# Kernel tuning notes

Hardware: AMD Instinct MI355X
Metric: run time of the kernel (lower is better)

Reference implementation:

```python
import jax, jax.numpy as jnp
import numpy as np

N, E, F, H, G, C = 50000, 800000, 128, 64, 512, 10
RATIO = 0.5  # forward arg `ratio` baked as constant


def seg_mean(msgs, idx, n):
    s = jax.ops.segment_sum(msgs, idx, num_segments=n)
    cnt = jax.ops.segment_sum(jnp.ones(idx.shape[0], msgs.dtype), idx, num_segments=n)
    return s / jnp.maximum(cnt, 1.0)[:, None]


def sage(x, src, dst, Wl, bl, Wr, ew=None):
    # PyG SAGEConv: lin_l(mean_{j->i} msg_j) + lin_r(x_i); weighted variant scales messages
    m = x[src] if ew is None else x[src] * ew[:, None]
    agg = seg_mean(m, dst, x.shape[0])
    return agg @ Wl + bl + x @ Wr


def topk_mask(scores, seg, num_graphs, ratio):
    # per-graph (segment) top-k edge selection: keep ceil(ratio*edges_in_graph) highest scores
    e = scores.shape[0]
    counts = jax.ops.segment_sum(jnp.ones(e, jnp.float32), seg, num_segments=num_graphs)
    order = jnp.lexsort((-scores, seg))  # sort by segment, then score descending
    seg_sorted = seg[order]
    starts = jnp.concatenate([jnp.zeros(1, jnp.float32), jnp.cumsum(counts)[:-1]])
    rank = jnp.arange(e, dtype=jnp.float32) - starts[seg_sorted]
    k = jnp.ceil(ratio * counts)
    sel = (rank < k[seg_sorted]).astype(scores.dtype)
    return jnp.zeros(e, scores.dtype).at[order].set(sel)


def setup_inputs():
    key = jax.random.key(0)
    ks = jax.random.split(key, 16)
    w = lambda k, shape, fan: (jax.random.normal(k, shape, jnp.float32) / np.sqrt(fan))
    return {
        'x': jax.random.normal(ks[0], (N, F), jnp.float32),
        'edge_index': jax.random.randint(ks[1], (2, E), 0, N, jnp.int32),
        'batch': jnp.sort(jax.random.randint(ks[2], (N,), 0, G, jnp.int32)),
        'W1l': w(ks[3], (F, H), F), 'b1l': jnp.zeros(H, jnp.float32), 'W1r': w(ks[4], (F, H), F),
        'W2l': w(ks[5], (H, H), H), 'b2l': jnp.zeros(H, jnp.float32), 'W2r': w(ks[6], (H, H), H),
        'W3l': w(ks[7], (H, H), H), 'b3l': jnp.zeros(H, jnp.float32), 'W3r': w(ks[8], (H, H), H),
        'Wlin1': w(ks[9], (H, H), H), 'blin1': jnp.zeros(H, jnp.float32),
        'Wlin2': w(ks[10], (H, C), H), 'blin2': jnp.zeros(C, jnp.float32),
    }


def reference(x, edge_index, batch, W1l, b1l, W1r, W2l, b2l, W2r, W3l, b3l, W3r, Wlin1, blin1, Wlin2, blin2):
    src, dst = edge_index[0], edge_index[1]
    h = jax.nn.relu(sage(x, src, dst, W1l, b1l, W1r))
    edge_scores = jnp.sum(h[src] * h[dst], axis=-1)  # [E]
    seg = batch[src]  # graph id per edge (sections)
    sampled = topk_mask(edge_scores, seg, G, RATIO)
    ew = edge_scores * sampled
    h = jax.nn.relu(sage(h, src, dst, W2l, b2l, W2r, ew))
    h = jax.nn.relu(sage(h, src, dst, W3l, b3l, W3r, ew))
    pooled = seg_mean(h, batch, G)  # global_mean_pool
    z = jax.nn.relu(pooled @ Wlin1 + blin1)
    z = z @ Wlin2 + blin2  # dropout inactive in eval
    return jax.nn.log_softmax(z, axis=-1), sampled
```

## Files before the change

kernel.cpp:

```cpp
#include <hip/hip_runtime.h>
#include <hip/hip_bf16.h>
#include <math.h>

static constexpr int N = 50000;
static constexpr int E = 800000;
static constexpr int F = 128;
static constexpr int H = 64;
static constexpr int G = 512;
static constexpr int C = 10;
static constexpr int CAP = 256;
static constexpr int NWIN = 8;
static constexpr int FILL_CH = 1280;
static constexpr int FB = E / FILL_CH;
static constexpr int DEGB = 256;
static constexpr int GB2 = (N + 31) / 32;
static constexpr int SB = E / 256;

static inline int cdiv(long a, int b) { return (int)((a + b - 1) / b); }

__device__ __forceinline__ float uinv_score(unsigned u) {
  return (u & 0x80000000u) ? __uint_as_float(u & 0x7fffffffu) : __uint_as_float(~u);
}

__device__ __forceinline__ int2 pack_slot(int s, int d, int g, int e) {
  unsigned a = (unsigned)s | ((unsigned)(d & 0x7FFF) << 17);
  unsigned b = ((unsigned)d >> 15) | ((unsigned)g << 2) | ((unsigned)e << 11);
  return make_int2((int)a, (int)b);
}
__device__ __forceinline__ int slot_src(int2 p) { return p.x & 0x1FFFF; }
__device__ __forceinline__ int slot_dst(int2 p) {
  return (int)(((unsigned)p.x >> 17) | (((unsigned)p.y & 3u) << 15));
}
__device__ __forceinline__ int slot_g(int2 p) { return (int)(((unsigned)p.y >> 2) & 0x1FFu); }
__device__ __forceinline__ int slot_eid(int2 p) { return (int)((unsigned)p.y >> 11); }

__global__ void k_deg_gemm(const int* __restrict__ dst, const int* __restrict__ batch,
                           int* __restrict__ deg, int* __restrict__ goff,
                           const float* __restrict__ x, const float* __restrict__ Wl,
                           const float* __restrict__ Wr, const float* __restrict__ bl,
                           float* __restrict__ y, float* __restrict__ r) {
  __shared__ float sx[16][F];
  int lane = threadIdx.x, ty = threadIdx.y;
  int tid = ty * 64 + lane;
  if (blockIdx.x >= DEGB) {
    int row0 = (blockIdx.x - DEGB) * 16;
    const float4* gsrc = (const float4*)(x + (size_t)row0 * F);
    float4* sdst = (float4*)(&sx[0][0]);
#pragma unroll
    for (int i = tid; i < 16 * F / 4; i += 256) sdst[i] = gsrc[i];
    __syncthreads();
    float al[4], ar[4];
    float bias = bl[lane];
#pragma unroll
    for (int j = 0; j < 4; ++j) { al[j] = 0.f; ar[j] = bias; }
#pragma unroll 4
    for (int f = 0; f < F; ++f) {
      float wl = Wl[f * H + lane];
      float wr = Wr[f * H + lane];
#pragma unroll
      for (int j = 0; j < 4; ++j) {
        float xv = sx[ty * 4 + j][f];
        al[j] += xv * wl;
        ar[j] += xv * wr;
      }
    }
#pragma unroll
    for (int j = 0; j < 4; ++j) {
      int row = row0 + ty * 4 + j;
      y[(size_t)row * H + lane] = al[j];
      r[(size_t)row * H + lane] = ar[j];
    }
    return;
  }
  for (int i = blockIdx.x * 256 + tid; i < N; i += DEGB * 256) {
    int b = batch[i];
    if (i == 0) {
      for (int g = 0; g <= b; ++g) goff[g] = 0;
    } else {
      int p = batch[i - 1];
      for (int g = p + 1; g <= b; ++g) goff[g] = i;
    }
    if (i == N - 1) {
      for (int g = b + 1; g <= G; ++g) goff[g] = N;
    }
  }
  const int4* d4 = (const int4*)dst;
  for (int i = blockIdx.x * 256 + tid; i < E / 4; i += DEGB * 256) {
    int4 v = d4[i];
    atomicAdd(&deg[v.x], 1);
    atomicAdd(&deg[v.y], 1);
    atomicAdd(&deg[v.z], 1);
    atomicAdd(&deg[v.w], 1);
  }
}

__global__ void k_scan_a(const int* __restrict__ cnt, int* __restrict__ off,
                         int* __restrict__ bsum, int n) {
  __shared__ int wsum[16];
  int tid = threadIdx.x, lane = tid & 63, wv = tid >> 6;
  int idx = blockIdx.x * 4096 + tid * 4;
  int v0 = (idx + 0 < n) ? cnt[idx + 0] : 0;
  int v1 = (idx + 1 < n) ? cnt[idx + 1] : 0;
  int v2 = (idx + 2 < n) ? cnt[idx + 2] : 0;
  int v3 = (idx + 3 < n) ? cnt[idx + 3] : 0;
  int local = v0 + v1 + v2 + v3;
  int inc = local;
  for (int d = 1; d < 64; d <<= 1) {
    int t = __shfl_up(inc, d);
    if (lane >= d) inc += t;
  }
  if (lane == 63) wsum[wv] = inc;
  __syncthreads();
  if (tid < 16) {
    int t = wsum[tid];
    for (int d = 1; d < 16; d <<= 1) {
      int u = __shfl_up(t, d);
      if (tid >= d) t += u;
    }
    wsum[tid] = t;
  }
  __syncthreads();
  int woff = (wv > 0) ? wsum[wv - 1] : 0;
  int excl = woff + inc - local;
  if (idx + 0 < n) off[idx + 0] = excl;
  if (idx + 1 < n) off[idx + 1] = excl + v0;
  if (idx + 2 < n) off[idx + 2] = excl + v0 + v1;
  if (idx + 3 < n) off[idx + 3] = excl + v0 + v1 + v2;
  if (tid == 0) bsum[blockIdx.x] = wsum[15];
}

__global__ void k_scan_c(int* __restrict__ off, int* __restrict__ cursor,
                         const int* __restrict__ bsum, int n, int nb) {
  __shared__ int spre[34];
  int tid = threadIdx.x;
  if (tid < 32) {
    int v = (tid < nb) ? bsum[tid] : 0;
    int inc = v;
    for (int d = 1; d < 32; d <<= 1) {
      int t = __shfl_up(inc, d);
      if (tid >= d) inc += t;
    }
    spre[tid] = inc - v;
  }
  __syncthreads();
  int i = blockIdx.x * 256 + tid;
  if (i < n) {
    int v = off[i] + spre[i >> 12];
    off[i] = v;
    cursor[i] = v;
  } else if (i == n) {
    off[n] = spre[nb];
  }
}

__global__ void k_fill(const int* __restrict__ src, const int* __restrict__ dst,
                       const int* __restrict__ batch, int* __restrict__ cursor,
                       int2* __restrict__ csrp, int* __restrict__ einv) {
  int win = blockIdx.x & 7;
  int chunk = blockIdx.x >> 3;
  int lo = win * (N / NWIN), hi = lo + (N / NWIN);
  int base = chunk * FILL_CH + threadIdx.x;
  int dd[FILL_CH / 256];
#pragma unroll
  for (int it = 0; it < FILL_CH / 256; ++it) dd[it] = dst[base + it * 256];
#pragma unroll
  for (int it = 0; it < FILL_CH / 256; ++it) {
    int d = dd[it];
    if (d >= lo && d < hi) {
      int e = base + it * 256;
      int s = src[e];
      int g = batch[s];
      int slot = atomicAdd(&cursor[d], 1);
      csrp[slot] = pack_slot(s, d, g, e);
      einv[e] = slot;
    }
  }
}

template <int K>
__global__ void k_gemm2h(const float* __restrict__ in, const float* __restrict__ Wl,
                         const float* __restrict__ Wr, const float* __restrict__ b,
                         __hip_bfloat16* __restrict__ y, float* __restrict__ r) {
  __shared__ float sx[16][K];
  int lane = threadIdx.x, ty = threadIdx.y;
  int tid = ty * 64 + lane;
  int row0 = blockIdx.x * 16;
  const float4* gsrc = (const float4*)(in + (size_t)row0 * K);
  float4* sdst = (float4*)(&sx[0][0]);
#pragma unroll
  for (int i = tid; i < 16 * K / 4; i += 256) sdst[i] = gsrc[i];
  __syncthreads();
  float al[4], ar[4];
  float bias = b[lane];
#pragma unroll
  for (int j = 0; j < 4; ++j) { al[j] = 0.f; ar[j] = bias; }
#pragma unroll 4
  for (int f = 0; f < K; ++f) {
    float wl = Wl[f * H + lane];
    float wr = Wr[f * H + lane];
#pragma unroll
    for (int j = 0; j < 4; ++j) {
      float xv = sx[ty * 4 + j][f];
      al[j] += xv * wl;
      ar[j] += xv * wr;
    }
  }
#pragma unroll
  for (int j = 0; j < 4; ++j) {
    int row = row0 + ty * 4 + j;
    y[(size_t)row * H + lane] = __float2bfloat16(al[j]);
    r[(size_t)row * H + lane] = ar[j];
  }
}

__global__ void k_agg1(const float* __restrict__ y, const float* __restrict__ r,
                       const int2* __restrict__ csrp, const int* __restrict__ off,
                       float* __restrict__ out) {
  int node = blockIdx.x * 8 + threadIdx.y;
  int lane = threadIdx.x;
  int q = lane >> 3, c = lane & 7;
  int s0 = off[node], s1 = off[node + 1];
  float4 a0 = make_float4(0.f, 0.f, 0.f, 0.f);
  float4 a1 = make_float4(0.f, 0.f, 0.f, 0.f);
  int i = s0 + q;
  for (; i + 8 < s1; i += 16) {
    int se0 = slot_src(csrp[i]);
    int se1 = slot_src(csrp[i + 8]);
    const float4* p0 = (const float4*)(y + (size_t)se0 * H);
    const float4* p1 = (const float4*)(y + (size_t)se1 * H);
    float4 u0 = p0[c], v0 = p0[c + 8];
    float4 u1 = p1[c], v1 = p1[c + 8];
    a0.x += u0.x + u1.x; a0.y += u0.y + u1.y; a0.z += u0.z + u1.z; a0.w += u0.w + u1.w;
    a1.x += v0.x + v1.x; a1.y += v0.y + v1.y; a1.z += v0.z + v1.z; a1.w += v0.w + v1.w;
  }
  for (; i < s1; i += 8) {
    int se = slot_src(csrp[i]);
    const float4* p = (const float4*)(y + (size_t)se * H);
    float4 u = p[c], v = p[c + 8];
    a0.x += u.x; a0.y += u.y; a0.z += u.z; a0.w += u.w;
    a1.x += v.x; a1.y += v.y; a1.z += v.z; a1.w += v.w;
  }
#pragma unroll
  for (int d = 8; d < 64; d <<= 1) {
    a0.x += __shfl_xor(a0.x, d); a0.y += __shfl_xor(a0.y, d);
    a0.z += __shfl_xor(a0.z, d); a0.w += __shfl_xor(a0.w, d);
    a1.x += __shfl_xor(a1.x, d); a1.y += __shfl_xor(a1.y, d);
    a1.w += __shfl_xor(a1.w, d); a1.z += __shfl_xor(a1.z, d);
  }
  if (q == 0) {
    float inv = 1.f / fmaxf((float)(s1 - s0), 1.f);
    const float4* rp = (const float4*)(r + (size_t)node * H);
    float4 r0 = rp[c], r1 = rp[c + 8];
    float4 o0, o1;
    o0.x = fmaxf(a0.x * inv + r0.x, 0.f); o0.y = fmaxf(a0.y * inv + r0.y, 0.f);
    o0.z = fmaxf(a0.z * inv + r0.z, 0.f); o0.w = fmaxf(a0.w * inv + r0.w, 0.f);
    o1.x = fmaxf(a1.x * inv + r1.x, 0.f); o1.y = fmaxf(a1.y * inv + r1.y, 0.f);
    o1.z = fmaxf(a1.z * inv + r1.z, 0.f); o1.w = fmaxf(a1.w * inv + r1.w, 0.f);
    float4* op = (float4*)(out + (size_t)node * H);
    op[c] = o0; op[c + 8] = o1;
  }
}

__global__ void k_agg_w(const __hip_bfloat16* __restrict__ y, const float* __restrict__ r,
                        const int2* __restrict__ csr2, const int* __restrict__ cnt2,
                        const int* __restrict__ off, float* __restrict__ out) {
  int node = blockIdx.x * 8 + threadIdx.y;
  int lane = threadIdx.x;
  int q = lane >> 3, c = lane & 7;
  int b0 = off[node], cn = cnt2[node];
  float a[8] = {0.f, 0.f, 0.f, 0.f, 0.f, 0.f, 0.f, 0.f};
  for (int j = q; j < cn; j += 8) {
    int2 sw = csr2[b0 + j];
    float w = __int_as_float(sw.y);
    uint4 pk = ((const uint4*)((const unsigned short*)y + (size_t)sw.x * H))[c];
    a[0] += w * __uint_as_float(pk.x << 16); a[1] += w * __uint_as_float(pk.x & 0xffff0000u);
    a[2] += w * __uint_as_float(pk.y << 16); a[3] += w * __uint_as_float(pk.y & 0xffff0000u);
    a[4] += w * __uint_as_float(pk.z << 16); a[5] += w * __uint_as_float(pk.z & 0xffff0000u);
    a[6] += w * __uint_as_float(pk.w << 16); a[7] += w * __uint_as_float(pk.w & 0xffff0000u);
  }
#pragma unroll
  for (int d = 8; d < 64; d <<= 1) {
#pragma unroll
    for (int j = 0; j < 8; ++j) a[j] += __shfl_xor(a[j], d);
  }
  if (q == 0) {
    int degn = off[node + 1] - off[node];
    float inv = 1.f / fmaxf((float)degn, 1.f);
    const float4* rp = (const float4*)(r + (size_t)node * H);
    float4 r0 = rp[2 * c], r1 = rp[2 * c + 1];
    float4 o0, o1;
    o0.x = fmaxf(a[0] * inv + r0.x, 0.f); o0.y = fmaxf(a[1] * inv + r0.y, 0.f);
    o0.z = fmaxf(a[2] * inv + r0.z, 0.f); o0.w = fmaxf(a[3] * inv + r0.w, 0.f);
    o1.x = fmaxf(a[4] * inv + r1.x, 0.f); o1.y = fmaxf(a[5] * inv + r1.y, 0.f);
    o1.z = fmaxf(a[6] * inv + r1.z, 0.f); o1.w = fmaxf(a[7] * inv + r1.w, 0.f);
    float4* op = (float4*)(out + (size_t)node * H);
    op[2 * c] = o0; op[2 * c + 1] = o1;
  }
}

__global__ void k_score_g2h(const float* __restrict__ h1, const int2* __restrict__ csrp,
                            unsigned* __restrict__ scoreu_csr,
                            unsigned short* __restrict__ seg_csr, int* __restrict__ hist,
                            const float* __restrict__ Wl, const float* __restrict__ Wr,
                            const float* __restrict__ bl,
                            __hip_bfloat16* __restrict__ y, float* __restrict__ r) {
  __shared__ float sx[32][H];
  int lane = threadIdx.x, ty = threadIdx.y;
  int q3 = blockIdx.x / 3, r3 = blockIdx.x - q3 * 3;
  if (r3 == 0 && q3 < GB2) {
    int tid = ty * 64 + lane;
    int row0 = q3 * 32;
    {
      int row = row0 + (tid >> 4);
      if (row < N)
        ((float4*)(&sx[0][0]))[tid] = ((const float4*)h1)[(size_t)row * (H / 4) + (tid & 15)];
    }
    __syncthreads();
    float al[4], ar[4];
    float bias = bl[lane];
#pragma unroll
    for (int j = 0; j < 4; ++j) { al[j] = 0.f; ar[j] = bias; }
#pragma unroll 4
    for (int f = 0; f < H; ++f) {
      float wl = Wl[f * H + lane];
      float wr = Wr[f * H + lane];
#pragma unroll
      for (int j = 0; j < 4; ++j) {
        float xv = sx[ty * 4 + j][f];
        al[j] += xv * wl;
        ar[j] += xv * wr;
      }
    }
#pragma unroll
    for (int j = 0; j < 4; ++j) {
      int row = row0 + ty * 4 + j;
      if (row < N) {
        y[(size_t)row * H + lane] = __float2bfloat16(al[j]);
        r[(size_t)row * H + lane] = ar[j];
      }
    }
  } else {
    int sid = blockIdx.x - (q3 + (r3 > 0 ? 1 : 0));
    int q = lane >> 4, c = lane & 15;
    int s = (sid * 8 + ty) * 32 + q * 8;
    int2 se[8];
#pragma unroll
    for (int j = 0; j < 8; ++j) se[j] = csrp[s + j];
    float4 xr[8], yr[8];
#pragma unroll
    for (int j = 0; j < 8; ++j)
      xr[j] = ((const float4*)(h1 + (size_t)slot_src(se[j]) * H))[c];
#pragma unroll
    for (int j = 0; j < 8; ++j)
      yr[j] = ((const float4*)(h1 + (size_t)slot_dst(se[j]) * H))[c];
    float p[8];
#pragma unroll
    for (int j = 0; j < 8; ++j)
      p[j] = yr[j].x * xr[j].x + yr[j].y * xr[j].y + yr[j].z * xr[j].z + yr[j].w * xr[j].w;
#pragma unroll
    for (int d = 1; d < 16; d <<= 1) {
#pragma unroll
      for (int j = 0; j < 8; ++j) p[j] += __shfl_xor(p[j], d);
    }
    if (c == 0) {
#pragma unroll
      for (int j = 0; j < 8; ++j) {
        int g = slot_g(se[j]);
        unsigned u = __float_as_uint(p[j]);
        u = (u & 0x80000000u) ? ~u : (u | 0x80000000u);
        scoreu_csr[s + j] = u;
        seg_csr[s + j] = (unsigned short)g;
        atomicAdd(&hist[g * 256 + (int)(u >> 24)], 1);
      }
    }
  }
}

__global__ void k_hist(const unsigned* __restrict__ scoreu, const unsigned short* __restrict__ seg,
                       const unsigned* __restrict__ prefix, int* __restrict__ hist, int pass) {
  int e = (blockIdx.x * 256 + threadIdx.x) * 4;
  if (e >= E) return;
  uint4 u4 = *(const uint4*)(scoreu + e);
  ushort4 s4 = *(const ushort4*)(seg + e);
  unsigned uu[4] = {u4.x, u4.y, u4.z, u4.w};
  int gg[4] = {(int)s4.x, (int)s4.y, (int)s4.z, (int)s4.w};
  int predshift = 32 - 8 * pass;
  int bshift = 24 - 8 * pass;
#pragma unroll
  for (int j = 0; j < 4; ++j) {
    unsigned u = uu[j];
    int g = gg[j];
    if ((u >> predshift) == (prefix[g] >> predshift))
      atomicAdd(&hist[g * 256 + (int)((u >> bshift) & 0xFFu)], 1);
  }
}

__global__ void k_scan(int* __restrict__ hist, unsigned* __restrict__ prefix,
                       int* __restrict__ krem, int pass) {
  int g = blockIdx.x;
  int lane = threadIdx.x;
  int4* row = (int4*)(hist + (size_t)g * 256);
  int4 v = row[lane];
  int vj[4] = {v.x, v.y, v.z, v.w};
  int s = v.x + v.y + v.z + v.w;
  int inc = s;
  for (int d = 1; d < 64; d <<= 1) {
    int t = __shfl_up(inc, d);
    if (lane >= d) inc += t;
  }
  int T = __shfl(inc, 63);
  int k = (pass == 0) ? ((T + 1) >> 1) : krem[g];
  int excl = inc - s;
  int pre[4] = {excl, excl + vj[0], excl + vj[0] + vj[1], excl + vj[0] + vj[1] + vj[2]};
  int bsel_l = -1, newk_l = 0;
  if (k > 0) {
    for (int j = 3; j >= 0; --j) {
      int suf = T - pre[j];
      if (suf >= k) { bsel_l = 4 * lane + j; newk_l = k - (suf - vj[j]); break; }
    }
  }
  unsigned long long mask = __ballot(bsel_l >= 0);
  int bsel = 255, newk = 0;
  if (k > 0 && mask) {
    int hi = 63 - __builtin_clzll(mask);
    bsel = __shfl(bsel_l, hi);
    newk = __shfl(newk_l, hi);
  }
  if (lane == 0) {
    unsigned base = (pass == 0) ? 0u : prefix[g];
    prefix[g] = base | ((unsigned)bsel << (24 - 8 * pass));
    krem[g] = newk;
  }
  row[lane] = make_int4(0, 0, 0, 0);
}

__global__ void k_select(const unsigned* __restrict__ scoreu_csr,
                         const unsigned short* __restrict__ seg_csr,
                         const unsigned* __restrict__ thresh,
                         int* __restrict__ eqcnt, int* __restrict__ eqlist,
                         unsigned char* __restrict__ sel_csr, float* __restrict__ ew_csr) {
  int s = (blockIdx.x * 256 + threadIdx.x) * 4;
  if (s >= E) return;
  uint4 u4 = *(const uint4*)(scoreu_csr + s);
  ushort4 g4 = *(const ushort4*)(seg_csr + s);
  unsigned uu[4] = {u4.x, u4.y, u4.z, u4.w};
  int gg[4] = {(int)g4.x, (int)g4.y, (int)g4.z, (int)g4.w};
  float ew[4];
  unsigned char sl[4];
#pragma unroll
  for (int j = 0; j < 4; ++j) {
    unsigned u = uu[j];
    int g = gg[j];
    unsigned t = thresh[g];
    unsigned um = u & 0xffffff00u;
    float sel = 0.f;
    if (um > t) sel = 1.f;
    else if (um == t) {
      int slot = atomicAdd(&eqcnt[g], 1);
      if (slot < CAP) eqlist[g * CAP + slot] = s + j;
    }
    sl[j] = (unsigned char)sel;
    ew[j] = uinv_score(u) * sel;
  }
  *(uchar4*)(sel_csr + s) = make_uchar4(sl[0], sl[1], sl[2], sl[3]);
  *(float4*)(ew_csr + s) = make_float4(ew[0], ew[1], ew[2], ew[3]);
}

__global__ void k_resolve(const int* __restrict__ krem, const int* __restrict__ eqcnt,
                          const int* __restrict__ eqlist, const int2* __restrict__ csrp,
                          const unsigned* __restrict__ scoreu_csr,
                          unsigned char* __restrict__ sel_csr, float* __restrict__ ew_csr) {
  int g = blockIdx.x * 256 + threadIdx.x;
  if (g >= G) return;
  int c = eqcnt[g]; if (c > CAP) c = CAP;
  int r = krem[g];  if (r > c) r = c;
  const int* lst = eqlist + g * CAP;
  unsigned last_u = 0u; int last_e = -1; bool first = true;
  for (int i = 0; i < r; ++i) {
    unsigned bu = 0u; int be = -1, bs = -1;
    for (int j = 0; j < c; ++j) {
      int slot = lst[j];
      unsigned u = scoreu_csr[slot];
      int eid = slot_eid(csrp[slot]);
      bool after = first || (u < last_u) || (u == last_u && eid > last_e);
      if (after && (bs < 0 || u > bu || (u == bu && eid < be))) { bu = u; be = eid; bs = slot; }
    }
    if (bs < 0) break;
    sel_csr[bs] = 1;
    ew_csr[bs] = uinv_score(bu);
    last_u = bu; last_e = be; first = false;
  }
}

__global__ void k_samp_comp(const unsigned char* __restrict__ sel,
                            const int2* __restrict__ csrp, const float* __restrict__ ewc,
                            const int* __restrict__ off, int2* __restrict__ csr2,
                            int* __restrict__ cnt2,
                            const int* __restrict__ einv, float* __restrict__ sampled) {
  int lane = threadIdx.x, ty = threadIdx.y;
  if (blockIdx.x < N / 8) {
    int node = blockIdx.x * 8 + ty;
    int s0 = off[node], s1 = off[node + 1];
    unsigned long long lt = ((unsigned long long)1 << lane) - 1;
    int cum = 0;
    for (int i0 = s0; i0 < s1; i0 += 64) {
      int i = i0 + lane;
      bool f = (i < s1) && sel[i];
      unsigned long long m = __ballot(f);
      if (f) {
        int rank = __popcll(m & lt);
        csr2[s0 + cum + rank] = make_int2(slot_src(csrp[i]), __float_as_int(ewc[i]));
      }
      cum += __popcll(m);
    }
    if (lane == 0) cnt2[node] = cum;
  } else {
    int tid = ty * 64 + lane;
    int e = ((blockIdx.x - N / 8) * 512 + tid) * 4;
    if (e >= E) return;
    int4 iv = *(const int4*)(einv + e);
    float4 o;
    o.x = (float)sel[iv.x];
    o.y = (float)sel[iv.y];
    o.z = (float)sel[iv.z];
    o.w = (float)sel[iv.w];
    *(float4*)(sampled + e) = o;
  }
}

__global__ void k_poolhead(const float* __restrict__ h3, const int* __restrict__ goff,
                           const float* __restrict__ W1, const float* __restrict__ b1,
                           const float* __restrict__ W2, const float* __restrict__ b2,
                           float* __restrict__ outp) {
  int g = blockIdx.x;
  int tid = threadIdx.x;
  int h = tid & 63, j = tid >> 6;
  int s0 = goff[g], s1 = goff[g + 1];
  float a = 0.f;
  for (int n = s0 + j; n < s1; n += 8) a += h3[(size_t)n * H + h];
  __shared__ float sp[8][H];
  __shared__ float p[H], z1[H], z2[C];
  __shared__ float lse;
  sp[j][h] = a;
  __syncthreads();
  if (j == 0) {
    float s = sp[0][h] + sp[1][h] + sp[2][h] + sp[3][h]
            + sp[4][h] + sp[5][h] + sp[6][h] + sp[7][h];
    float inv = 1.f / fmaxf((float)(s1 - s0), 1.f);
    p[h] = s * inv;
  }
  __syncthreads();
  if (j == 0) {
    float acc = b1[h];
#pragma unroll 8
    for (int f = 0; f < H; ++f) acc += p[f] * W1[f * H + h];
    z1[h] = fmaxf(acc, 0.f);
  }
  __syncthreads();
  if (tid < C) {
    float a2 = b2[tid];
#pragma unroll 8
    for (int f = 0; f < H; ++f) a2 += z1[f] * W2[f * C + tid];
    z2[tid] = a2;
  }
  __syncthreads();
  if (tid == 0) {
    float m = z2[0];
    for (int c = 1; c < C; ++c) m = fmaxf(m, z2[c]);
    float s = 0.f;
    for (int c = 0; c < C; ++c) s += expf(z2[c] - m);
    lse = m + logf(s);
  }
  __syncthreads();
  if (tid < C) outp[(size_t)g * C + tid] = z2[tid] - lse;
}

extern "C" void kernel_launch(void* const* d_in, const int* in_sizes, int n_in,
                              void* d_out, int out_size, void* d_ws, size_t ws_size,
                              hipStream_t stream) {
  const float* x     = (const float*)d_in[0];
  const int*   ei    = (const int*)d_in[1];
  const int*   batch = (const int*)d_in[2];
  const float* W1l   = (const float*)d_in[3];
  const float* b1l   = (const float*)d_in[4];
  const float* W1r   = (const float*)d_in[5];
  const float* W2l   = (const float*)d_in[6];
  const float* b2l   = (const float*)d_in[7];
  const float* W2r   = (const float*)d_in[8];
  const float* W3l   = (const float*)d_in[9];
  const float* b3l   = (const float*)d_in[10];
  const float* W3r   = (const float*)d_in[11];
  const float* Wlin1 = (const float*)d_in[12];
  const float* blin1 = (const float*)d_in[13];
  const float* Wlin2 = (const float*)d_in[14];
  const float* blin2 = (const float*)d_in[15];

  const int* srcv = ei;
  const int* dstv = ei + E;

  float* out_ls   = (float*)d_out;
  float* out_samp = out_ls + G * C;

  char* w = (char*)d_ws;
  auto carve = [&](size_t bytes) { void* p = (void*)w; w += (bytes + 255) & ~(size_t)255; return p; };
  char* zbase   = w;
  int*      deg     = (int*)carve((size_t)N * 4);
  int*      eqcnt   = (int*)carve((size_t)G * 4);
  int*      hist    = (int*)carve((size_t)G * 256 * 4);
  size_t    zbytes  = (size_t)(w - zbase);
  float*    h1      = (float*)carve((size_t)N * H * 4);
  float*    h2      = (float*)carve((size_t)N * H * 4);
  float*    h3      = (float*)carve((size_t)N * H * 4);
  float*    yb      = (float*)carve((size_t)N * H * 4);
  float*    rb      = (float*)carve((size_t)N * H * 4);
  __hip_bfloat16* ybh = (__hip_bfloat16*)carve((size_t)N * H * 2);
  unsigned* scoreu_csr = (unsigned*)carve((size_t)E * 4);
  unsigned short* seg_csr = (unsigned short*)carve((size_t)E * 2);
  float*    ew_csr     = (float*)carve((size_t)E * 4);
  unsigned char* sel_csr = (unsigned char*)carve((size_t)E);
  int2*     csrp    = (int2*)carve((size_t)E * 8);
  int*      einv    = (int*)carve((size_t)E * 4);
  int*      off     = (int*)carve((size_t)(N + 1) * 4);
  int*      cursor  = (int*)carve((size_t)N * 4);
  int*      cnt2    = (int*)carve((size_t)N * 4);
  int*      goff    = (int*)carve((size_t)(G + 1) * 4);
  unsigned* prefix  = (unsigned*)carve((size_t)G * 4);
  int*      krem    = (int*)carve((size_t)G * 4);
  int*      eqlist  = (int*)carve((size_t)G * CAP * 4);
  int*      bsum    = (int*)carve((size_t)16 * 4);
  int2*     csr2    = (int2*)carve((size_t)E * 8);

  hipMemsetAsync(zbase, 0, zbytes, stream);

  k_deg_gemm<<<DEGB + N / 16, dim3(64, 4), 0, stream>>>(dstv, batch, deg, goff,
                                                        x, W1l, W1r, b1l, yb, rb);
  int nb = cdiv(N, 4096);
  k_scan_a<<<nb, 1024, 0, stream>>>(deg, off, bsum, N);
  k_scan_c<<<cdiv(N + 1, 256), 256, 0, stream>>>(off, cursor, bsum, N, nb);

  k_fill<<<8 * FB, 256, 0, stream>>>(srcv, dstv, batch, cursor, csrp, einv);

  k_agg1<<<N / 8, dim3(64, 8), 0, stream>>>(yb, rb, csrp, off, h1);

  k_score_g2h<<<SB + GB2, dim3(64, 8), 0, stream>>>(h1, csrp, scoreu_csr, seg_csr, hist,
                                                    W2l, W2r, b2l, ybh, rb);
  k_scan<<<G, 64, 0, stream>>>(hist, prefix, krem, 0);
  for (int p = 1; p <= 2; ++p) {
    k_hist<<<cdiv(E / 4, 256), 256, 0, stream>>>(scoreu_csr, seg_csr, prefix, hist, p);
    k_scan<<<G, 64, 0, stream>>>(hist, prefix, krem, p);
  }
  k_select<<<cdiv(E / 4, 256), 256, 0, stream>>>(scoreu_csr, seg_csr, prefix,
                                                 eqcnt, eqlist, sel_csr, ew_csr);
  k_resolve<<<cdiv(G, 256), 256, 0, stream>>>(krem, eqcnt, eqlist, csrp, scoreu_csr,
                                              sel_csr, ew_csr);

  k_samp_comp<<<N / 8 + cdiv(E / 4, 512), dim3(64, 8), 0, stream>>>(
      sel_csr, csrp, ew_csr, off, csr2, cnt2, einv, out_samp);

  k_agg_w<<<N / 8, dim3(64, 8), 0, stream>>>(ybh, rb, csr2, cnt2, off, h2);

  k_gemm2h<H><<<N / 16, dim3(64, 4), 0, stream>>>(h2, W3l, W3r, b3l, ybh, rb);
  k_agg_w<<<N / 8, dim3(64, 8), 0, stream>>>(ybh, rb, csr2, cnt2, off, h3);

  k_poolhead<<<G, 512, 0, stream>>>(h3, goff, Wlin1, blin1, Wlin2, blin2, out_ls);
}
```

Measured before the change: 436.9 us.

## Move layer-1 GEMM into fill kernel and window degree atomics by dst range

The layer-1 dense GEMM blocks move out of the degree-count kernel and into the CSR fill kernel, so the GEMM runs alongside the atomic-heavy fill instead of the degree pass. The degree kernel now uses 512 blocks split into 8 destination windows, each block atomically incrementing only degrees in its window. The aim is to improve atomic locality and let the memory-bound fill overlap with compute. In exchange, each window rereads the whole dst array, and the fill kernel grows in size and shared-memory use.

```diff
diff --git a/kernel.cpp b/kernel.cpp
--- a/kernel.cpp
+++ b/kernel.cpp
@@ -12,7 +12,7 @@
 static constexpr int NWIN = 8;
 static constexpr int FILL_CH = 1280;
 static constexpr int FB = E / FILL_CH;
-static constexpr int DEGB = 256;
+static constexpr int DEGB = 512;
 static constexpr int GB2 = (N + 31) / 32;
 static constexpr int SB = E / 256;
 
@@ -34,44 +34,9 @@
 __device__ __forceinline__ int slot_g(int2 p) { return (int)(((unsigned)p.y >> 2) & 0x1FFu); }
 __device__ __forceinline__ int slot_eid(int2 p) { return (int)((unsigned)p.y >> 11); }
 
-__global__ void k_deg_gemm(const int* __restrict__ dst, const int* __restrict__ batch,
-                           int* __restrict__ deg, int* __restrict__ goff,
-                           const float* __restrict__ x, const float* __restrict__ Wl,
-                           const float* __restrict__ Wr, const float* __restrict__ bl,
-                           float* __restrict__ y, float* __restrict__ r) {
-  __shared__ float sx[16][F];
-  int lane = threadIdx.x, ty = threadIdx.y;
-  int tid = ty * 64 + lane;
-  if (blockIdx.x >= DEGB) {
-    int row0 = (blockIdx.x - DEGB) * 16;
-    const float4* gsrc = (const float4*)(x + (size_t)row0 * F);
-    float4* sdst = (float4*)(&sx[0][0]);
-#pragma unroll
-    for (int i = tid; i < 16 * F / 4; i += 256) sdst[i] = gsrc[i];
-    __syncthreads();
-    float al[4], ar[4];
-    float bias = bl[lane];
-#pragma unroll
-    for (int j = 0; j < 4; ++j) { al[j] = 0.f; ar[j] = bias; }
-#pragma unroll 4
-    for (int f = 0; f < F; ++f) {
-      float wl = Wl[f * H + lane];
-      float wr = Wr[f * H + lane];
-#pragma unroll
-      for (int j = 0; j < 4; ++j) {
-        float xv = sx[ty * 4 + j][f];
-        al[j] += xv * wl;
-        ar[j] += xv * wr;
-      }
-    }
-#pragma unroll
-    for (int j = 0; j < 4; ++j) {
-      int row = row0 + ty * 4 + j;
-      y[(size_t)row * H + lane] = al[j];
-      r[(size_t)row * H + lane] = ar[j];
-    }
-    return;
-  }
+__global__ void k_deg_goff(const int* __restrict__ dst, const int* __restrict__ batch,
+                           int* __restrict__ deg, int* __restrict__ goff) {
+  int tid = threadIdx.x;
   for (int i = blockIdx.x * 256 + tid; i < N; i += DEGB * 256) {
     int b = batch[i];
     if (i == 0) {
@@ -84,13 +49,16 @@
       for (int g = b + 1; g <= G; ++g) goff[g] = N;
     }
   }
+  int win = blockIdx.x & 7;
+  int wb = blockIdx.x >> 3;
+  int lo = win * (N / NWIN), hi = lo + (N / NWIN);
   const int4* d4 = (const int4*)dst;
-  for (int i = blockIdx.x * 256 + tid; i < E / 4; i += DEGB * 256) {
+  for (int i = wb * 256 + tid; i < E / 4; i += (DEGB / 8) * 256) {
     int4 v = d4[i];
-    atomicAdd(&deg[v.x], 1);
-    atomicAdd(&deg[v.y], 1);
-    atomicAdd(&deg[v.z], 1);
-    atomicAdd(&deg[v.w], 1);
+    if (v.x >= lo && v.x < hi) atomicAdd(&deg[v.x], 1);
+    if (v.y >= lo && v.y < hi) atomicAdd(&deg[v.y], 1);
+    if (v.z >= lo && v.z < hi) atomicAdd(&deg[v.z], 1);
+    if (v.w >= lo && v.w < hi) atomicAdd(&deg[v.w], 1);
   }
 }
 
@@ -153,27 +121,63 @@
   }
 }
 
-__global__ void k_fill(const int* __restrict__ src, const int* __restrict__ dst,
-                       const int* __restrict__ batch, int* __restrict__ cursor,
-                       int2* __restrict__ csrp, int* __restrict__ einv) {
-  int win = blockIdx.x & 7;
-  int chunk = blockIdx.x >> 3;
-  int lo = win * (N / NWIN), hi = lo + (N / NWIN);
-  int base = chunk * FILL_CH + threadIdx.x;
-  int dd[FILL_CH / 256];
-#pragma unroll
-  for (int it = 0; it < FILL_CH / 256; ++it) dd[it] = dst[base + it * 256];
-#pragma unroll
-  for (int it = 0; it < FILL_CH / 256; ++it) {
-    int d = dd[it];
-    if (d >= lo && d < hi) {
-      int e = base + it * 256;
-      int s = src[e];
-      int g = batch[s];
-      int slot = atomicAdd(&cursor[d], 1);
-      csrp[slot] = pack_slot(s, d, g, e);
-      einv[e] = slot;
-    }
+__global__ void k_fill_gemm(const int* __restrict__ src, const int* __restrict__ dst,
+                            const int* __restrict__ batch, int* __restrict__ cursor,
+                            int2* __restrict__ csrp, int* __restrict__ einv,
+                            const float* __restrict__ x, const float* __restrict__ Wl,
+                            const float* __restrict__ Wr, const float* __restrict__ bl,
+                            float* __restrict__ y, float* __restrict__ r) {
+  __shared__ float sx[16][F];
+  int lane = threadIdx.x, ty = threadIdx.y;
+  int tid = ty * 64 + lane;
+  if (blockIdx.x < 8 * FB) {
+    int win = blockIdx.x & 7;
+    int chunk = blockIdx.x >> 3;
+    int lo = win * (N / NWIN), hi = lo + (N / NWIN);
+    int base = chunk * FILL_CH + tid;
+    int dd[FILL_CH / 256];
+#pragma unroll
+    for (int it = 0; it < FILL_CH / 256; ++it) dd[it] = dst[base + it * 256];
+#pragma unroll
+    for (int it = 0; it < FILL_CH / 256; ++it) {
+      int d = dd[it];
+      if (d >= lo && d < hi) {
+        int e = base + it * 256;
+        int s = src[e];
+        int g = batch[s];
+        int slot = atomicAdd(&cursor[d], 1);
+        csrp[slot] = pack_slot(s, d, g, e);
+        einv[e] = slot;
+      }
+    }
+    return;
+  }
+  int row0 = (blockIdx.x - 8 * FB) * 16;
+  const float4* gsrc = (const float4*)(x + (size_t)row0 * F);
+  float4* sdst = (float4*)(&sx[0][0]);
+#pragma unroll
+  for (int i = tid; i < 16 * F / 4; i += 256) sdst[i] = gsrc[i];
+  __syncthreads();
+  float al[4], ar[4];
+  float bias = bl[lane];
+#pragma unroll
+  for (int j = 0; j < 4; ++j) { al[j] = 0.f; ar[j] = bias; }
+#pragma unroll 4
+  for (int f = 0; f < F; ++f) {
+    float wl = Wl[f * H + lane];
+    float wr = Wr[f * H + lane];
+#pragma unroll
+    for (int j = 0; j < 4; ++j) {
+      float xv = sx[ty * 4 + j][f];
+      al[j] += xv * wl;
+      ar[j] += xv * wr;
+    }
+  }
+#pragma unroll
+  for (int j = 0; j < 4; ++j) {
+    int row = row0 + ty * 4 + j;
+    y[(size_t)row * H + lane] = al[j];
+    r[(size_t)row * H + lane] = ar[j];
   }
 }
 
@@ -245,7 +249,7 @@
     a0.x += __shfl_xor(a0.x, d); a0.y += __shfl_xor(a0.y, d);
     a0.z += __shfl_xor(a0.z, d); a0.w += __shfl_xor(a0.w, d);
     a1.x += __shfl_xor(a1.x, d); a1.y += __shfl_xor(a1.y, d);
-    a1.w += __shfl_xor(a1.w, d); a1.z += __shfl_xor(a1.z, d);
+    a1.z += __shfl_xor(a1.z, d); a1.w += __shfl_xor(a1.w, d);
   }
   if (q == 0) {
     float inv = 1.f / fmaxf((float)(s1 - s0), 1.f);
@@ -632,13 +636,14 @@
 
   hipMemsetAsync(zbase, 0, zbytes, stream);
 
-  k_deg_gemm<<<DEGB + N / 16, dim3(64, 4), 0, stream>>>(dstv, batch, deg, goff,
-                                                        x, W1l, W1r, b1l, yb, rb);
+  k_deg_goff<<<DEGB, 256, 0, stream>>>(dstv, batch, deg, goff);
   int nb = cdiv(N, 4096);
   k_scan_a<<<nb, 1024, 0, stream>>>(deg, off, bsum, N);
   k_scan_c<<<cdiv(N + 1, 256), 256, 0, stream>>>(off, cursor, bsum, N, nb);
 
-  k_fill<<<8 * FB, 256, 0, stream>>>(srcv, dstv, batch, cursor, csrp, einv);
+  k_fill_gemm<<<8 * FB + N / 16, dim3(64, 4), 0, stream>>>(srcv, dstv, batch, cursor,
+                                                           csrp, einv,
+                                                           x, W1l, W1r, b1l, yb, rb);
 
   k_agg1<<<N / 8, dim3(64, 8), 0, stream>>>(yb, rb, csrp, off, h1);
 
```

New measurement: 432.1 us. About the same (-1.1%).
